# Performance work log

Measured on AMD Instinct MI355X. Metric: run time of the kernel, lower is better.

The kernel has to match this reference:

```python
import jax, jax.numpy as jnp
import numpy as np
import math

B, S, D, O_DIM = 8, 2048, 1024, 1024

def setup_inputs() -> dict:
    key = jax.random.key(0)
    ks = jax.random.split(key, 4)
    scale = 1.0 / math.sqrt(D)
    return {
        "x": jax.random.normal(ks[0], (B, S, D), dtype=jnp.float32),
        "Wq": jax.random.normal(ks[1], (D, O_DIM), dtype=jnp.float32) * scale,
        "bq": jnp.zeros((O_DIM,), dtype=jnp.float32),
        "Wk": jax.random.normal(ks[2], (D, O_DIM), dtype=jnp.float32) * scale,
        "bk": jnp.zeros((O_DIM,), dtype=jnp.float32),
        "Wv": jax.random.normal(ks[3], (D, O_DIM), dtype=jnp.float32) * scale,
        "bv": jnp.zeros((O_DIM,), dtype=jnp.float32),
    }

def reference(x, Wq, bq, Wk, bk, Wv, bv):
    o_dim = Wq.shape[1]
    q = x @ Wq + bq  # [B,S,O]
    k = x @ Wk + bk
    v = x @ Wv + bv
    scores = jnp.einsum('bid,bjd->bij', q, k) / jnp.sqrt(jnp.float32(o_dim))
    n = scores.shape[1]
    # causal additive mask: upper triangle (j > i) gets -1e20 added
    causal = jnp.tril(jnp.ones((n, n), dtype=scores.dtype))
    scores = scores + (1.0 - causal) * (-1e20)
    probs = jax.nn.softmax(scores, axis=-1)
    return jnp.einsum('bij,bjd->bid', probs, v)
```

## Files before the change

kernel.cpp:

```cpp
#include <hip/hip_runtime.h>

#define BM 128
#define BN 128
#define BK 32

typedef unsigned short u16;
typedef unsigned int u32;
typedef __attribute__((ext_vector_type(8))) short short8;
typedef __attribute__((ext_vector_type(4))) float floatx4;

__device__ __forceinline__ u16 f2bf(float f) {
  u32 u = __float_as_uint(f);
  return (u16)((u + 0x7FFFu + ((u >> 16) & 1u)) >> 16);
}

__device__ __forceinline__ float bf2f(u16 b) {
  return __uint_as_float(((u32)b) << 16);
}

__device__ __forceinline__ void gload16(const void* g, void* l) {
  __builtin_amdgcn_global_load_lds((const __attribute__((address_space(1))) void*)g,
                                   (__attribute__((address_space(3))) void*)l, 16, 0, 0);
}

template<int BIAS_MODE, bool OUT_BF16, bool CAUSAL, bool KLIMIT, int SWZ>
__global__ __launch_bounds__(256)
void gemm_nt(const u16* __restrict__ A, int lda, long strideA,
             const u16* __restrict__ B, int ldb, long strideB,
             void* __restrict__ Cv, int ldc, long strideC,
             const float* __restrict__ bias, float scale,
             int M, int N, int K)
{
  int bx = blockIdx.x;
  int by = blockIdx.y;
  if (SWZ == 1) {
    const int c = gridDim.x >> 3;
    bx = (bx & 7) * c + (bx >> 3);
  } else if (SWZ == 2) {
    const u32 gx = gridDim.x;
    const u32 flat = (u32)by * gx + (u32)bx;
    const u32 j = flat & 7u;
    const u32 w = flat >> 3;
    const u32 rpx = gridDim.y >> 3;
    by = (int)(j * rpx + w / gx);
    bx = (int)(w % gx);
  } else if (SWZ == 3) {
    by = gridDim.y - 1 - by;
  }
  const int rb = by * BM;
  const int cb = bx * BN;
  if (CAUSAL && cb > rb + (BM - 1)) return;

  A += (long)blockIdx.z * strideA;
  B += (long)blockIdx.z * strideB;
  const long coff = (long)blockIdx.z * strideC;

  __shared__ u16 As[BM * BK];
  __shared__ u16 Bs[BN * BK];

  const int t = threadIdx.x;
  const int lane = t & 63;
  const int wid = t >> 6;
  const int wr = wid >> 1, wc = wid & 1;

  floatx4 acc[4][4];
#pragma unroll
  for (int i = 0; i < 4; ++i)
#pragma unroll
    for (int j = 0; j < 4; ++j) acc[i][j] = (floatx4)(0.0f);

  const int srow = t >> 2;
  const int schunk = (t & 3) ^ ((srow >> 1) & 3);
  const u16* Ag0 = A + (long)(rb + srow) * lda + schunk * 8;
  const u16* Ag1 = A + (long)(rb + srow + 64) * lda + schunk * 8;
  const u16* Bg0 = B + (long)(cb + srow) * ldb + schunk * 8;
  const u16* Bg1 = B + (long)(cb + srow + 64) * ldb + schunk * 8;
  char* AsW = (char*)As + wid * 1024;
  char* BsW = (char*)Bs + wid * 1024;

  const int arow = wr * 64 + (lane & 15);
  const int brow = wc * 64 + (lane & 15);
  const int rchunk = lane >> 4;
  int aoff[4], boff[4];
#pragma unroll
  for (int i = 0; i < 4; ++i) {
    const int ra = arow + i * 16;
    aoff[i] = ra * 64 + ((rchunk ^ ((ra >> 1) & 3)) * 16);
    const int rbq = brow + i * 16;
    boff[i] = rbq * 64 + ((rchunk ^ ((rbq >> 1) & 3)) * 16);
  }

  int kend = K;
  if (KLIMIT) kend = (rb + BM < K) ? (rb + BM) : K;
  const int ktiles = kend / BK;

  for (int kt = 0; kt < ktiles; ++kt) {
    const long ko = (long)kt * BK;
    gload16(Ag0 + ko, AsW);
    gload16(Ag1 + ko, AsW + 4096);
    gload16(Bg0 + ko, BsW);
    gload16(Bg1 + ko, BsW + 4096);
    __syncthreads();
    short8 af[4], bfr[4];
#pragma unroll
    for (int i = 0; i < 4; ++i) {
      af[i]  = *(const short8*)((const char*)As + aoff[i]);
      bfr[i] = *(const short8*)((const char*)Bs + boff[i]);
    }
#pragma unroll
    for (int mi = 0; mi < 4; ++mi)
#pragma unroll
      for (int nj = 0; nj < 4; ++nj)
        acc[mi][nj] = __builtin_amdgcn_mfma_f32_16x16x32_bf16(af[mi], bfr[nj], acc[mi][nj], 0, 0, 0);
    __syncthreads();
  }

#pragma unroll
  for (int mi = 0; mi < 4; ++mi) {
    const int r0 = rb + wr * 64 + mi * 16 + (lane >> 4) * 4;
#pragma unroll
    for (int nj = 0; nj < 4; ++nj) {
      const int c = cb + wc * 64 + nj * 16 + (lane & 15);
      float bc = 0.0f;
      if (BIAS_MODE == 1) bc = bias[c];
#pragma unroll
      for (int e = 0; e < 4; ++e) {
        const int r = r0 + e;
        float val = acc[mi][nj][e] * scale + bc;
        if (BIAS_MODE == 2) val += bias[r];
        const long idx = coff + (long)r * ldc + c;
        if (OUT_BF16) ((u16*)Cv)[idx] = f2bf(val);
        else          ((float*)Cv)[idx] = val;
      }
    }
  }
}

__global__ __launch_bounds__(256)
void softmax_causal_bf16(u16* __restrict__ Pp, int n, long stride)
{
  const int i = blockIdx.x;
  u16* row = Pp + (long)blockIdx.y * stride + (long)i * n;
  const int t = threadIdx.x;
  const int lane = t & 63, wid = t >> 6;
  const int jb = t * 8;

  float v[8];
  const bool any = (jb <= i);
  if (any) {
    short8 sv = *(const short8*)(row + jb);
#pragma unroll
    for (int e = 0; e < 8; ++e) v[e] = bf2f((u16)sv[e]);
  } else {
#pragma unroll
    for (int e = 0; e < 8; ++e) v[e] = 0.0f;
  }

  float mx = -3.0e38f;
#pragma unroll
  for (int e = 0; e < 8; ++e) if (any && jb + e <= i) mx = fmaxf(mx, v[e]);
#pragma unroll
  for (int off = 32; off > 0; off >>= 1) mx = fmaxf(mx, __shfl_xor(mx, off));
  __shared__ float red[8];
  if (lane == 0) red[wid] = mx;
  __syncthreads();
  mx = fmaxf(fmaxf(red[0], red[1]), fmaxf(red[2], red[3]));

  float s = 0.0f;
#pragma unroll
  for (int e = 0; e < 8; ++e) {
    float p = (any && jb + e <= i) ? __expf(v[e] - mx) : 0.0f;
    v[e] = p; s += p;
  }
#pragma unroll
  for (int off = 32; off > 0; off >>= 1) s += __shfl_xor(s, off);
  if (lane == 0) red[4 + wid] = s;
  __syncthreads();
  s = red[4] + red[5] + red[6] + red[7];
  const float inv = 1.0f / s;

  short8 o;
#pragma unroll
  for (int e = 0; e < 8; ++e) o[e] = (short)f2bf(v[e] * inv);
  *(short8*)(row + jb) = o;
}

__global__ __launch_bounds__(256)
void transpose_conv(const float* __restrict__ W, u16* __restrict__ WT, int dim)
{
  __shared__ float tile[32][33];
  const int tx = threadIdx.x & 31;
  const int ty = threadIdx.x >> 5;
  const int c0 = blockIdx.x * 32;
  const int r0 = blockIdx.y * 32;
#pragma unroll
  for (int i = 0; i < 4; ++i)
    tile[ty + 8 * i][tx] = W[(long)(r0 + ty + 8 * i) * dim + c0 + tx];
  __syncthreads();
#pragma unroll
  for (int i = 0; i < 4; ++i)
    WT[(long)(c0 + ty + 8 * i) * dim + r0 + tx] = f2bf(tile[tx][ty + 8 * i]);
}

__global__ __launch_bounds__(256)
void conv_bf16(const float* __restrict__ X, u16* __restrict__ Xb, long n8)
{
  const long i = (long)blockIdx.x * 256 + threadIdx.x;
  if (i >= n8) return;
  const float4* s = (const float4*)X + i * 2;
  float4 a = s[0], b = s[1];
  short8 o;
  o[0] = (short)f2bf(a.x); o[1] = (short)f2bf(a.y);
  o[2] = (short)f2bf(a.z); o[3] = (short)f2bf(a.w);
  o[4] = (short)f2bf(b.x); o[5] = (short)f2bf(b.y);
  o[6] = (short)f2bf(b.z); o[7] = (short)f2bf(b.w);
  ((short8*)Xb)[i] = o;
}

__global__ __launch_bounds__(256)
void pack_bias2(const float* __restrict__ b0, const float* __restrict__ b1,
                float* __restrict__ dst, int n)
{
  const int i = blockIdx.x * 256 + threadIdx.x;
  if (i < n) dst[i] = b0[i];
  else if (i < 2 * n) dst[i] = b1[i - n];
}

extern "C" void kernel_launch(void* const* d_in, const int* in_sizes, int n_in,
                              void* d_out, int out_size, void* d_ws, size_t ws_size,
                              hipStream_t stream)
{
  const int Bb = 8, S = 2048, Dd = 1024, Od = 1024;
  const int M = Bb * S;

  const float* x  = (const float*)d_in[0];
  const float* Wq = (const float*)d_in[1];
  const float* bq = (const float*)d_in[2];
  const float* Wk = (const float*)d_in[3];
  const float* bk = (const float*)d_in[4];
  const float* Wv = (const float*)d_in[5];
  const float* bv = (const float*)d_in[6];
  float* out = (float*)d_out;

  char* ws = (char*)d_ws;
  u16* xb   = (u16*)(ws);
  u16* qk   = (u16*)(ws + 33554432L);
  u16* vT   = (u16*)(ws + 100663296L);
  u16* WqkT = (u16*)(ws + 134217728L);
  u16* WvT  = (u16*)(ws + 138412032L);
  float* bqk = (float*)(ws + 140509184L);
  const size_t attn_base = 140517376UL;

  conv_bf16<<<dim3(8192), dim3(256), 0, stream>>>(x, xb, (long)M * Dd / 8);
  transpose_conv<<<dim3(32, 32), dim3(256), 0, stream>>>(Wq, WqkT, Dd);
  transpose_conv<<<dim3(32, 32), dim3(256), 0, stream>>>(Wk, WqkT + (long)Od * Dd, Dd);
  transpose_conv<<<dim3(32, 32), dim3(256), 0, stream>>>(Wv, WvT, Dd);
  pack_bias2<<<dim3(8), dim3(256), 0, stream>>>(bq, bk, bqk, Od);

  dim3 blk(256);
  gemm_nt<1, true, false, false, 2><<<dim3(2 * Od / BN, M / BM, 1), blk, 0, stream>>>(
      xb, Dd, 0L, WqkT, Dd, 0L, qk, 2 * Od, 0L, bqk, 1.0f, M, 2 * Od, Dd);
  gemm_nt<2, true, false, false, 1><<<dim3(M / BN, Od / BM, 1), blk, 0, stream>>>(
      WvT, Dd, 0L, xb, Dd, 0L, vT, M, 0L, bv, 1.0f, Od, M, Dd);

  const u16* qb = qk;
  const u16* kb = qk + Od;
  const int ldqk = 2 * Od;
  const long strideQK = (long)S * ldqk;
  const long sS = (long)S * S;

  u16* scores;
  int g;
  if (ws_size >= attn_base + 8UL * (size_t)sS * sizeof(u16)) {
    scores = (u16*)(ws + attn_base);
    g = 8;
  } else {
    scores = xb;
    g = 4;
  }

  const float sc = 0.03125f;
  for (int b0 = 0; b0 < Bb; b0 += g) {
    const int gz = (b0 + g <= Bb) ? g : (Bb - b0);
    gemm_nt<0, true, true, false, 0><<<dim3(S / BN, S / BM, gz), blk, 0, stream>>>(
        qb + (long)b0 * strideQK, ldqk, strideQK,
        kb + (long)b0 * strideQK, ldqk, strideQK,
        scores, S, sS, nullptr, sc, S, S, Od);
    softmax_causal_bf16<<<dim3(S, gz), blk, 0, stream>>>(scores, S, sS);
    gemm_nt<0, false, false, true, 3><<<dim3(Od / BN, S / BM, gz), blk, 0, stream>>>(
        scores, S, sS, vT + (long)b0 * S, M, (long)S,
        out + (long)b0 * S * Od, Od, (long)S * Od, nullptr, 1.0f, S, Od, S);
  }
}
```

Before: 474.3 us.

## Add 256x256-tile 512-thread GEMM kernel for QKV projections

Adds a new bf16 MFMA GEMM kernel that uses 256x256 output tiles, 8 waves per block and a 4-deep global-to-LDS pipeline over 128KB of shared memory. It replaces the 128x128 GEMM for the Q/K and V projection launches. The goal is more operand reuse per loaded byte and more overlap of loads with MFMA work. The cost is much higher register and LDS use per block, which lowers occupancy, and fewer blocks in the grid. The attention GEMMs still use the old kernel.

```diff
diff --git a/kernel.cpp b/kernel.cpp
--- a/kernel.cpp
+++ b/kernel.cpp
@@ -21,6 +21,142 @@
 __device__ __forceinline__ void gload16(const void* g, void* l) {
   __builtin_amdgcn_global_load_lds((const __attribute__((address_space(1))) void*)g,
                                    (__attribute__((address_space(3))) void*)l, 16, 0, 0);
+}
+
+template<int BIAS_MODE, int SWZ>
+__global__ __launch_bounds__(512, 2)
+void gemm256(const u16* __restrict__ A, int lda,
+             const u16* __restrict__ B, int ldb,
+             u16* __restrict__ C, int ldc,
+             const float* __restrict__ bias, int K)
+{
+  int bx = blockIdx.x, by = blockIdx.y;
+  if (SWZ == 1) {
+    const int c = gridDim.x >> 3;
+    bx = (bx & 7) * c + (bx >> 3);
+  } else if (SWZ == 2) {
+    const u32 gx = gridDim.x;
+    const u32 flat = (u32)by * gx + (u32)bx;
+    const u32 j = flat & 7u, w = flat >> 3;
+    const u32 rpx = gridDim.y >> 3;
+    by = (int)(j * rpx + w / gx);
+    bx = (int)(w % gx);
+  }
+  const int rb = by * 256, cb = bx * 256;
+
+  __shared__ __align__(16) char lds[131072];
+
+  const int t = threadIdx.x;
+  const int lane = t & 63, wid = t >> 6;
+  const int wr = wid >> 2, wc = wid & 3;
+
+  floatx4 acc[8][4];
+#pragma unroll
+  for (int i = 0; i < 8; ++i)
+#pragma unroll
+    for (int j = 0; j < 4; ++j) acc[i][j] = (floatx4)(0.0f);
+
+  const int sr = t >> 2;
+  const int sl = (t & 3) ^ ((sr >> 1) & 3);
+  const u16* Ag0 = A + (long)(rb + sr) * lda + sl * 8;
+  const u16* Ag1 = A + (long)(rb + sr + 128) * lda + sl * 8;
+  const u16* Bg0 = B + (long)(cb + sr) * ldb + sl * 8;
+  const u16* Bg1 = B + (long)(cb + sr + 128) * ldb + sl * 8;
+
+#define STAGE_A(T) { const long ko_ = (long)(T) * 32;                          \
+    char* d_ = lds + (((T) & 3) << 15) + (wid << 10);                          \
+    gload16(Ag0 + ko_, d_); gload16(Ag1 + ko_, d_ + 8192); }
+#define STAGE_B(T) { const long ko_ = (long)(T) * 32;                          \
+    char* d_ = lds + (((T) & 3) << 15) + 16384 + (wid << 10);                  \
+    gload16(Bg0 + ko_, d_); gload16(Bg1 + ko_, d_ + 8192); }
+
+  const int g = lane >> 4;
+  int aoff[8], boff[4];
+  const int arow = wr * 128 + (lane & 15);
+  const int brow = wc * 64 + (lane & 15);
+#pragma unroll
+  for (int i = 0; i < 8; ++i) {
+    const int ra = arow + i * 16;
+    aoff[i] = ra * 64 + ((g ^ ((ra >> 1) & 3)) * 16);
+  }
+#pragma unroll
+  for (int j = 0; j < 4; ++j) {
+    const int rbq = brow + j * 16;
+    boff[j] = rbq * 64 + ((g ^ ((rbq >> 1) & 3)) * 16);
+  }
+
+  const int NT = K / 32;
+
+  STAGE_A(0); STAGE_B(0);
+  STAGE_A(1); STAGE_B(1);
+  STAGE_A(2); STAGE_B(2);
+  asm volatile("s_waitcnt vmcnt(8)" ::: "memory");
+  __builtin_amdgcn_s_barrier();
+  asm volatile("" ::: "memory");
+
+  for (int T = 0; T < NT; ++T) {
+    const char* bufA = lds + ((T & 3) << 15);
+    const char* bufB = bufA + 16384;
+
+    if (T + 3 < NT) STAGE_A(T + 3);
+    short8 a0[4], bfr[4];
+#pragma unroll
+    for (int i = 0; i < 4; ++i) a0[i] = *(const short8*)(bufA + aoff[i]);
+#pragma unroll
+    for (int j = 0; j < 4; ++j) bfr[j] = *(const short8*)(bufB + boff[j]);
+    __builtin_amdgcn_s_setprio(1);
+#pragma unroll
+    for (int mi = 0; mi < 4; ++mi)
+#pragma unroll
+      for (int nj = 0; nj < 4; ++nj)
+        acc[mi][nj] = __builtin_amdgcn_mfma_f32_16x16x32_bf16(a0[mi], bfr[nj], acc[mi][nj], 0, 0, 0);
+    __builtin_amdgcn_s_setprio(0);
+
+    if (T + 3 < NT) STAGE_B(T + 3);
+    short8 a1[4];
+#pragma unroll
+    for (int i = 0; i < 4; ++i) a1[i] = *(const short8*)(bufA + aoff[4 + i]);
+    __builtin_amdgcn_s_setprio(1);
+#pragma unroll
+    for (int mi = 0; mi < 4; ++mi)
+#pragma unroll
+      for (int nj = 0; nj < 4; ++nj)
+        acc[4 + mi][nj] = __builtin_amdgcn_mfma_f32_16x16x32_bf16(a1[mi], bfr[nj], acc[4 + mi][nj], 0, 0, 0);
+    __builtin_amdgcn_s_setprio(0);
+
+    asm volatile("" ::: "memory");
+    if (T < NT - 3) {
+      asm volatile("s_waitcnt vmcnt(8)" ::: "memory");
+      __builtin_amdgcn_s_barrier();
+    } else if (T == NT - 3) {
+      asm volatile("s_waitcnt vmcnt(4)" ::: "memory");
+      __builtin_amdgcn_s_barrier();
+    } else if (T == NT - 2) {
+      asm volatile("s_waitcnt vmcnt(0)" ::: "memory");
+      __builtin_amdgcn_s_barrier();
+    }
+    asm volatile("" ::: "memory");
+  }
+#undef STAGE_A
+#undef STAGE_B
+
+#pragma unroll
+  for (int mi = 0; mi < 8; ++mi) {
+    const int r0 = rb + wr * 128 + mi * 16 + (lane >> 4) * 4;
+#pragma unroll
+    for (int nj = 0; nj < 4; ++nj) {
+      const int c = cb + wc * 64 + nj * 16 + (lane & 15);
+      float bc = 0.0f;
+      if (BIAS_MODE == 1) bc = bias[c];
+#pragma unroll
+      for (int e = 0; e < 4; ++e) {
+        const int r = r0 + e;
+        float val = acc[mi][nj][e] + bc;
+        if (BIAS_MODE == 2) val += bias[r];
+        C[(long)r * ldc + c] = f2bf(val);
+      }
+    }
+  }
 }
 
 template<int BIAS_MODE, bool OUT_BF16, bool CAUSAL, bool KLIMIT, int SWZ>
@@ -257,11 +393,10 @@
   transpose_conv<<<dim3(32, 32), dim3(256), 0, stream>>>(Wv, WvT, Dd);
   pack_bias2<<<dim3(8), dim3(256), 0, stream>>>(bq, bk, bqk, Od);
 
-  dim3 blk(256);
-  gemm_nt<1, true, false, false, 2><<<dim3(2 * Od / BN, M / BM, 1), blk, 0, stream>>>(
-      xb, Dd, 0L, WqkT, Dd, 0L, qk, 2 * Od, 0L, bqk, 1.0f, M, 2 * Od, Dd);
-  gemm_nt<2, true, false, false, 1><<<dim3(M / BN, Od / BM, 1), blk, 0, stream>>>(
-      WvT, Dd, 0L, xb, Dd, 0L, vT, M, 0L, bv, 1.0f, Od, M, Dd);
+  gemm256<1, 2><<<dim3(2 * Od / 256, M / 256), dim3(512), 0, stream>>>(
+      xb, Dd, WqkT, Dd, qk, 2 * Od, bqk, Dd);
+  gemm256<2, 1><<<dim3(M / 256, Od / 256), dim3(512), 0, stream>>>(
+      WvT, Dd, xb, Dd, vT, M, bv, Dd);
 
   const u16* qb = qk;
   const u16* kb = qk + Od;
@@ -279,6 +414,7 @@
     g = 4;
   }
 
+  dim3 blk(256);
   const float sc = 0.03125f;
   for (int b0 = 0; b0 < Bb; b0 += g) {
     const int gz = (b0 + g <= Bb) ? g : (Bb - b0);
```

New measurement: 439.4 us. 1.08x faster.
